# Kernel tuning notes

Measured on AMD Instinct MI355X. Metric: run time of the kernel, lower is better.

## Reference

```python
import jax, jax.numpy as jnp
import numpy as np

B, SEQ, PRED, CIN, COUT = 4, 3584, 512, 7, 7
L = SEQ + PRED              # 4096, divisible by 2*BS -> fit_length is a no-op
D, H, DH, FF, EL = 512, 8, 64, 2048, 2
BS, NHASH = 64, 4           # bucket_size, n_hashes
NB = L // BS                # 64 buckets per hash round
SELF_ATTN_VAL = -5e4        # reformer_pytorch TOKEN_SELF_ATTN_VALUE


def layer_norm(x, g, b, eps=1e-5):
    m = jnp.mean(x, -1, keepdims=True)
    v = jnp.mean((x - m) ** 2, -1, keepdims=True)
    return (x - m) * jax.lax.rsqrt(v + eps) * g + b


def lsh_attention(qk, v, rot):
    # qk, v: (bh, L, DH); rot: (DH, NHASH, NB//2)  (shared across batch & heads)
    bh, Lx, dh = qk.shape
    nb = Lx // BS
    # --- hash vectors ---
    rv = jnp.einsum('btf,fhi->bhti', qk, rot)              # (bh, NHASH, L, nb//2)
    rv = jnp.concatenate([rv, -rv], axis=-1)
    buckets = jnp.argmax(rv, axis=-1)                      # (bh, NHASH, L) int
    buckets = buckets + (jnp.arange(NHASH) * nb)[None, :, None]
    buckets = buckets.reshape(bh, NHASH * Lx)
    ticker = jnp.arange(NHASH * Lx)
    bt = Lx * buckets + (ticker % Lx)[None]                # unique keys
    # --- sort by (bucket, position) ---
    sticker = jnp.argsort(bt, axis=-1)                     # (bh, NHASH*L)
    undo = jnp.argsort(sticker, axis=-1)
    st = sticker % Lx
    sqk = jnp.take_along_axis(qk, st[..., None], axis=1)   # (bh, NHASH*L, DH)
    sv = jnp.take_along_axis(v, st[..., None], axis=1)
    ch = NHASH * nb                                        # number of chunks
    bq_t = st.reshape(bh, ch, BS)
    bqk = sqk.reshape(bh, ch, BS, dh)
    bv = sv.reshape(bh, ch, BS, dh)
    bq = bqk
    nrm = jnp.sqrt(jnp.sum(bqk * bqk, -1, keepdims=True))
    bk = bqk / jnp.maximum(nrm, 1e-12)                     # F.normalize
    def look_one_back(t):
        prev = jnp.concatenate([t[:, -1:], t[:, :-1]], axis=1)
        return jnp.concatenate([t, prev], axis=2)
    bk = look_one_back(bk)
    bvv = look_one_back(bv)
    bkv_t = look_one_back(bq_t)
    dots = jnp.einsum('bcie,bcje->bcij', bq, bk) * (dh ** -0.5)  # (bh, ch, BS, 2BS)
    self_mask = bq_t[..., :, None] == bkv_t[..., None, :]
    dots = jnp.where(self_mask, SELF_ATTN_VAL, dots)
    lse = jax.scipy.special.logsumexp(dots, axis=-1, keepdims=True)
    p = jnp.exp(dots - lse)
    bo = jnp.einsum('bcij,bcje->bcie', p, bvv)
    so = bo.reshape(bh, NHASH * Lx, dh)
    slog = lse.reshape(bh, NHASH * Lx)
    o = jnp.take_along_axis(so, undo[..., None], axis=1)
    logits = jnp.take_along_axis(slog, undo, axis=1)
    o = o.reshape(bh, NHASH, Lx, dh)
    logits = logits.reshape(bh, NHASH, Lx, 1)
    probs = jnp.exp(logits - jax.scipy.special.logsumexp(logits, axis=1, keepdims=True))
    return jnp.sum(o * probs, axis=1)                      # (bh, L, DH)


def lsh_self_attention(x, Wqk, Wv, Wo, bo, rot):
    Bs, Lx, _ = x.shape
    qk = (x @ Wqk).reshape(Bs, Lx, H, DH).transpose(0, 2, 1, 3).reshape(Bs * H, Lx, DH)
    v = (x @ Wv).reshape(Bs, Lx, H, DH).transpose(0, 2, 1, 3).reshape(Bs * H, Lx, DH)
    out = lsh_attention(qk, v, rot)
    out = out.reshape(Bs, H, Lx, DH).transpose(0, 2, 1, 3).reshape(Bs, Lx, D)
    return out @ Wo + bo


def _forward(x_enc, x_dec, x_mark_enc, x_mark_dec, conv_w, month_emb, day_emb,
             weekday_emb, hour_emb, minute_emb, W_qk, W_v, W_out, b_out, rotations,
             ln1_g, ln1_b, W_ff1, b_ff1, W_ff2, b_ff2, ln2_g, ln2_b, lnf_g, lnf_b,
             W_proj, b_proj):
    x = jnp.concatenate([x_enc, x_dec[:, -PRED:, :]], axis=1)            # (B, L, CIN)
    xm = jnp.concatenate([x_mark_enc, x_mark_dec[:, -PRED:, :]], axis=1)
    # TokenEmbedding: Conv1d k=3, circular padding, no bias
    xp = jnp.concatenate([x[:, -1:], x, x[:, :1]], axis=1)
    tok = jax.lax.conv_general_dilated(xp, conv_w, (1,), 'VALID',
                                       dimension_numbers=('NWC', 'WIO', 'NWC'))
    # TemporalEmbedding (freq='t': month/day/weekday/hour/minute)
    temp = (month_emb[xm[..., 0]] + day_emb[xm[..., 1]] + weekday_emb[xm[..., 2]]
            + hour_emb[xm[..., 3]] + minute_emb[xm[..., 4]])
    # PositionalEmbedding (sinusoidal)
    pos = jnp.arange(L, dtype=jnp.float32)[:, None]
    div = jnp.exp(jnp.arange(0, D, 2, dtype=jnp.float32) * (-np.log(10000.0) / D))
    pe = jnp.zeros((L, D), jnp.float32).at[:, 0::2].set(jnp.sin(pos * div)).at[:, 1::2].set(jnp.cos(pos * div))
    h = tok + temp + pe[None]
    for l in range(EL):
        a = lsh_self_attention(h, W_qk[l], W_v[l], W_out[l], b_out[l], rotations[l])
        h = layer_norm(h + a, ln1_g[l], ln1_b[l])
        y = jax.nn.gelu(h @ W_ff1[l] + b_ff1[l], approximate=False)
        y = y @ W_ff2[l] + b_ff2[l]
        h = layer_norm(h + y, ln2_g[l], ln2_b[l])
    h = layer_norm(h, lnf_g, lnf_b)
    return h[:, -PRED:] @ W_proj + b_proj                  # (B, PRED, COUT)


def setup_inputs():
    ks = jax.random.split(jax.random.key(0), 20)
    def n(k, shape, fan_in):
        return jax.random.normal(k, shape, jnp.float32) / np.sqrt(fan_in)
    return {
        'x_enc': jax.random.normal(ks[0], (B, SEQ, CIN), jnp.float32),
        'x_dec': jax.random.normal(ks[1], (B, PRED, CIN), jnp.float32),
        'x_mark_enc': jax.random.randint(ks[2], (B, SEQ, 5), 0, 4, jnp.int32),
        'x_mark_dec': jax.random.randint(ks[3], (B, PRED, 5), 0, 4, jnp.int32),
        'conv_w': n(ks[4], (3, CIN, D), 3 * CIN),
        'month_emb': 0.02 * jax.random.normal(ks[5], (13, D), jnp.float32),
        'day_emb': 0.02 * jax.random.normal(ks[6], (32, D), jnp.float32),
        'weekday_emb': 0.02 * jax.random.normal(ks[7], (7, D), jnp.float32),
        'hour_emb': 0.02 * jax.random.normal(ks[8], (24, D), jnp.float32),
        'minute_emb': 0.02 * jax.random.normal(ks[9], (4, D), jnp.float32),
        'W_qk': n(ks[10], (EL, D, D), D),
        'W_v': n(ks[11], (EL, D, D), D),
        'W_out': n(ks[12], (EL, D, D), D),
        'b_out': jnp.zeros((EL, D), jnp.float32),
        'rotations': jax.random.normal(ks[13], (EL, DH, NHASH, NB // 2), jnp.float32),
        'ln1_g': jnp.ones((EL, D), jnp.float32),
        'ln1_b': jnp.zeros((EL, D), jnp.float32),
        'W_ff1': n(ks[14], (EL, D, FF), D),
        'b_ff1': jnp.zeros((EL, FF), jnp.float32),
        'W_ff2': n(ks[15], (EL, FF, D), FF),
        'b_ff2': jnp.zeros((EL, D), jnp.float32),
        'ln2_g': jnp.ones((EL, D), jnp.float32),
        'ln2_b': jnp.zeros((EL, D), jnp.float32),
        'lnf_g': jnp.ones((D,), jnp.float32),
        'lnf_b': jnp.zeros((D,), jnp.float32),
        'W_proj': n(ks[16], (D, COUT), D),
        'b_proj': jnp.zeros((COUT,), jnp.float32),
    }


def reference(x_enc, x_dec, x_mark_enc, x_mark_dec, conv_w, month_emb, day_emb,
              weekday_emb, hour_emb, minute_emb, W_qk, W_v, W_out, b_out, rotations,
              ln1_g, ln1_b, W_ff1, b_ff1, W_ff2, b_ff2, ln2_g, ln2_b, lnf_g, lnf_b,
              W_proj, b_proj):
    return _forward(x_enc, x_dec, x_mark_enc, x_mark_dec, conv_w, month_emb, day_emb,
                    weekday_emb, hour_emb, minute_emb, W_qk, W_v, W_out, b_out, rotations,
                    ln1_g, ln1_b, W_ff1, b_ff1, W_ff2, b_ff2, ln2_g, ln2_b, lnf_g, lnf_b,
                    W_proj, b_proj)
```

## Files before the change

kernel.cpp:

```cpp
#include <hip/hip_runtime.h>
#include <math.h>


typedef __attribute__((ext_vector_type(8))) __bf16 bf16x8;
typedef __attribute__((ext_vector_type(4))) float floatx4;

__device__ __forceinline__ unsigned short f2bf(float f) {
  union { float f; unsigned int u; } x; x.f = f;
  unsigned int r = x.u + 0x7fffu + ((x.u >> 16) & 1u);
  return (unsigned short)(r >> 16);
}
__device__ __forceinline__ float bf2f(unsigned short u) {
  union { unsigned int u; float f; } x; x.u = ((unsigned int)u) << 16;
  return x.f;
}
__device__ __forceinline__ float gelu_f(float x) {
  return 0.5f * x * (1.0f + erff(x * 0.70710678118654752440f));
}

__global__ __launch_bounds__(256) void pe_kernel(float* __restrict__ pe)
{
  int t = blockIdx.x;
#pragma unroll
  for (int rep = 0; rep < 2; ++rep) {
    int d = threadIdx.x + rep * 256;
    float cf = (float)(-9.210340371976184 / 512.0);
    float xf = (float)(d & ~1) * cf;
    float freq = (float)exp((double)xf);
    float angf = (float)t * freq;
    double a = (double)angf;
    pe[t * 512 + d] = (float)((d & 1) ? cos(a) : sin(a));
  }
}

__global__ __launch_bounds__(256) void embed_kernel(
    const float* __restrict__ x_enc, const float* __restrict__ x_dec,
    const int* __restrict__ xm_enc, const int* __restrict__ xm_dec,
    const float* __restrict__ conv_w,
    const float* __restrict__ month, const float* __restrict__ day,
    const float* __restrict__ wday, const float* __restrict__ hour,
    const float* __restrict__ minute, const float* __restrict__ pe,
    float* __restrict__ h)
{
  int idx = blockIdx.x;
  int b = idx >> 12, t = idx & 4095;
  __shared__ float xv[21];
  __shared__ int mi[5];
  int tid = threadIdx.x;
  if (tid < 21) {
    int w = tid / 7, c = tid % 7;
    int s = (t + w + 4095) & 4095;
    xv[tid] = (s < 3584) ? x_enc[(s + b*3584)*7 + c]
                         : x_dec[((s - 3584) + b*512)*7 + c];
  }
  if (tid >= 32 && tid < 37) {
    int j = tid - 32;
    mi[j] = (t < 3584) ? xm_enc[(b*3584 + t)*5 + j]
                       : xm_dec[(b*512 + (t - 3584))*5 + j];
  }
  __syncthreads();
  int m0 = mi[0], m1 = mi[1], m2 = mi[2], m3 = mi[3], m4 = mi[4];
#pragma unroll
  for (int rep = 0; rep < 2; ++rep) {
    int d = tid + rep*256;
    float tok = 0.f;
#pragma unroll
    for (int wc = 0; wc < 21; ++wc) tok += xv[wc] * conv_w[wc*512 + d];
    float temp = month[m0*512+d] + day[m1*512+d] + wday[m2*512+d]
               + hour[m3*512+d] + minute[m4*512+d];
    h[(size_t)idx*512 + d] = tok + temp + pe[t*512 + d];
  }
}

template<int ACT>
__global__ __launch_bounds__(256) void gemm_kernel(
    const float* __restrict__ A, const float* __restrict__ W,
    const float* __restrict__ bias, float* __restrict__ C,
    int M, int N, int K)
{
  __shared__ float As[8][132];
  __shared__ float Bs[8][132];
  int tid = threadIdx.x;
  int bm = blockIdx.x, bn = blockIdx.y;
  int tr = tid >> 4, tc = tid & 15;
  double acc[8][8];
  float tt[8][8];
#pragma unroll
  for (int i=0;i<8;++i)
#pragma unroll
    for (int j=0;j<8;++j) { acc[i][j]=0.0; tt[i][j]=0.f; }

  int am  = tid >> 1;
  int at  = (tid & 1) * 4;
  int bkr = tid >> 5;
  int bn4 = (tid & 31) * 4;
  const float* Aptr = A + (size_t)(bm*128 + am)*K + at;
  const float* Bptr = W + (size_t)bkr*N + bn*128 + bn4;

  int phase = 0;
  for (int k0 = 0; k0 < K; k0 += 8) {
    float4 a4 = *(const float4*)(Aptr + k0);
    float4 b4 = *(const float4*)(Bptr + (size_t)k0*N);
    __syncthreads();
    As[at+0][am] = a4.x; As[at+1][am] = a4.y;
    As[at+2][am] = a4.z; As[at+3][am] = a4.w;
    *(float4*)&Bs[bkr][bn4] = b4;
    __syncthreads();
#pragma unroll
    for (int k=0;k<8;++k) {
      float4 a0 = *(const float4*)&As[k][tr*8];
      float4 a1 = *(const float4*)&As[k][tr*8+4];
      float4 b0 = *(const float4*)&Bs[k][tc*8];
      float4 b1 = *(const float4*)&Bs[k][tc*8+4];
      float av[8] = {a0.x,a0.y,a0.z,a0.w,a1.x,a1.y,a1.z,a1.w};
      float bv[8] = {b0.x,b0.y,b0.z,b0.w,b1.x,b1.y,b1.z,b1.w};
#pragma unroll
      for (int i=0;i<8;++i)
#pragma unroll
        for (int j=0;j<8;++j) tt[i][j] += av[i]*bv[j];
    }
    phase ^= 1;
    if (!phase) {
#pragma unroll
      for (int i=0;i<8;++i)
#pragma unroll
        for (int j=0;j<8;++j) { acc[i][j] += (double)tt[i][j]; tt[i][j]=0.f; }
    }
  }
  int row0 = bm*128 + tr*8;
  int col0 = bn*128 + tc*8;
  float bvb[8];
#pragma unroll
  for (int j=0;j<8;++j) bvb[j] = bias ? bias[col0+j] : 0.f;
#pragma unroll
  for (int i=0;i<8;++i) {
    float o[8];
#pragma unroll
    for (int j=0;j<8;++j) {
      float vv = (float)acc[i][j] + bvb[j];
      if (ACT==1) vv = gelu_f(vv);
      o[j] = vv;
    }
    float4* dst = (float4*)(C + (size_t)(row0+i)*N + col0);
    dst[0] = make_float4(o[0],o[1],o[2],o[3]);
    dst[1] = make_float4(o[4],o[5],o[6],o[7]);
  }
}

template<int SPLIT>
__global__ __launch_bounds__(256) void wsplit_kernel(
    const float* __restrict__ W, unsigned short* __restrict__ Wt, int K, int N)
{
  __shared__ float tile[32][33];
  int k0 = blockIdx.x*32, n0 = blockIdx.y*32;
  int tid = threadIdx.x;
  int kk = tid >> 3, nn4 = (tid & 7)*4;
  float4 w4 = *(const float4*)(W + (size_t)(k0+kk)*N + n0 + nn4);
  tile[kk][nn4+0]=w4.x; tile[kk][nn4+1]=w4.y;
  tile[kk][nn4+2]=w4.z; tile[kk][nn4+3]=w4.w;
  __syncthreads();
  int n = tid >> 3, k4 = (tid & 7)*4;
  unsigned short o[3][4];
#pragma unroll
  for (int j=0;j<4;++j) {
    float v = tile[k4+j][n];
    unsigned short h0 = f2bf(v);
    float r = v - bf2f(h0);
    unsigned short h1 = f2bf(r);
    o[0][j] = h0; o[1][j] = h1;
    if (SPLIT==3) { float r2 = r - bf2f(h1); o[2][j] = f2bf(r2); }
  }
#pragma unroll
  for (int p=0;p<SPLIT;++p) {
    ushort4* d = (ushort4*)(Wt + (size_t)p*N*K + (size_t)(n0+n)*K + k0 + k4);
    *d = make_ushort4(o[p][0], o[p][1], o[p][2], o[p][3]);
  }
}

template<int SPLIT, int ACT>
__global__ __launch_bounds__(256, 3) void gemm_mfma(
    const float* __restrict__ A, const unsigned short* __restrict__ Wt,
    const float* __restrict__ bias, float* __restrict__ C,
    int M, int N, int K)
{
  constexpr int RS = SPLIT*32 + 8;
  __shared__ __align__(16) unsigned short smem[2*128*RS];
  unsigned short* sA = smem;
  unsigned short* sB = smem + 128*RS;
  float* sE = (float*)smem;

  int tid = threadIdx.x;
  int bm = blockIdx.x, bn = blockIdx.y;
  int lane = tid & 63, wave = tid >> 6;
  int wm = wave & 1, wn = wave >> 1;
  int fr = lane & 15, fk = (lane >> 4) * 8;

  floatx4 acc[4][4];
#pragma unroll
  for (int i=0;i<4;++i)
#pragma unroll
    for (int j=0;j<4;++j) acc[i][j] = (floatx4){0.f,0.f,0.f,0.f};

  int row = tid >> 1, kseg = (tid & 1) * 16;
  const float* aSrc = A + (size_t)(bm*128 + row)*K + kseg;
  const unsigned short* bSrc = Wt + (size_t)(bn*128 + row)*K + kseg;

  float4 av4[4];
  uint4 bv[SPLIT][2];
#pragma unroll
  for (int q=0;q<4;++q) av4[q] = *(const float4*)(aSrc + q*4);
#pragma unroll
  for (int p=0;p<SPLIT;++p) {
    const unsigned short* bp = bSrc + (size_t)p*N*K;
    bv[p][0] = *(const uint4*)(bp);
    bv[p][1] = *(const uint4*)(bp + 8);
  }

  for (int k0 = 0; k0 < K; k0 += 32) {
    __syncthreads();
    unsigned short us[SPLIT][16];
    const float* ff = (const float*)av4;
#pragma unroll
    for (int i=0;i<16;++i) {
      float v = ff[i];
      unsigned short h0 = f2bf(v);
      float r = v - bf2f(h0);
      us[0][i] = h0;
      unsigned short h1 = f2bf(r);
      us[1][i] = h1;
      if (SPLIT==3) { float r2 = r - bf2f(h1); us[2][i] = f2bf(r2); }
    }
#pragma unroll
    for (int p=0;p<SPLIT;++p) {
      uint4* d = (uint4*)&sA[row*RS + p*32 + kseg];
      d[0] = *(const uint4*)&us[p][0];
      d[1] = *(const uint4*)&us[p][8];
      uint4* db = (uint4*)&sB[row*RS + p*32 + kseg];
      db[0] = bv[p][0];
      db[1] = bv[p][1];
    }
    __syncthreads();
    if (k0 + 32 < K) {
#pragma unroll
      for (int q=0;q<4;++q) av4[q] = *(const float4*)(aSrc + k0 + 32 + q*4);
#pragma unroll
      for (int p=0;p<SPLIT;++p) {
        const unsigned short* bp = bSrc + (size_t)p*N*K + k0 + 32;
        bv[p][0] = *(const uint4*)(bp);
        bv[p][1] = *(const uint4*)(bp + 8);
      }
    }

    bf16x8 aF[4][SPLIT];
#pragma unroll
    for (int mt=0;mt<4;++mt)
#pragma unroll
      for (int p=0;p<SPLIT;++p)
        aF[mt][p] = *(const bf16x8*)&sA[(wm*64 + mt*16 + fr)*RS + p*32 + fk];
#pragma unroll
    for (int nt=0;nt<4;++nt) {
      bf16x8 bF[SPLIT];
#pragma unroll
      for (int p=0;p<SPLIT;++p)
        bF[p] = *(const bf16x8*)&sB[(wn*64 + nt*16 + fr)*RS + p*32 + fk];
#pragma unroll
      for (int mt=0;mt<4;++mt) {
        floatx4 c = acc[mt][nt];
        if (SPLIT==3) {
          c = __builtin_amdgcn_mfma_f32_16x16x32_bf16(aF[mt][2], bF[0], c, 0,0,0);
          c = __builtin_amdgcn_mfma_f32_16x16x32_bf16(aF[mt][1], bF[1], c, 0,0,0);
          c = __builtin_amdgcn_mfma_f32_16x16x32_bf16(aF[mt][0], bF[2], c, 0,0,0);
        }
        c = __builtin_amdgcn_mfma_f32_16x16x32_bf16(aF[mt][1], bF[0], c, 0,0,0);
        c = __builtin_amdgcn_mfma_f32_16x16x32_bf16(aF[mt][0], bF[1], c, 0,0,0);
        c = __builtin_amdgcn_mfma_f32_16x16x32_bf16(aF[mt][0], bF[0], c, 0,0,0);
        acc[mt][nt] = c;
      }
    }
  }

  __syncthreads();
#pragma unroll
  for (int half = 0; half < 2; ++half) {
    if (wm == half) {
#pragma unroll
      for (int nt=0;nt<4;++nt) {
        int cl = wn*64 + nt*16 + fr;
        float bb = bias ? bias[bn*128 + cl] : 0.f;
#pragma unroll
        for (int mt=0;mt<4;++mt) {
          int r0 = mt*16 + (lane>>4)*4;
#pragma unroll
          for (int j=0;j<4;++j) {
            float vv = acc[mt][nt][j] + bb;
            if (ACT==1) vv = gelu_f(vv);
            sE[(r0+j)*132 + cl] = vv;
          }
        }
      }
    }
    __syncthreads();
#pragma unroll
    for (int it=0; it<8; ++it) {
      int idx = it*256 + tid;
      int rr = idx >> 5, c4 = (idx & 31) * 4;
      float4 vv = *(const float4*)&sE[rr*132 + c4];
      *(float4*)(C + (size_t)(bm*128 + half*64 + rr)*N + bn*128 + c4) = vv;
    }
    __syncthreads();
  }
}

__global__ __launch_bounds__(256) void hash_kernel(
    const float* __restrict__ qk, const float* __restrict__ rot,
    unsigned char* __restrict__ buckets)
{
  __shared__ float q[2][64];
  __shared__ double rv[2][128];
  int half = threadIdx.x >> 7;
  int lt = threadIdx.x & 127;
  int g = blockIdx.x*2 + half;
  int bh = g >> 12, t = g & 4095;
  int b = bh >> 3, hd = bh & 7;
  if (lt < 64)
    q[half][lt] = qk[((size_t)(b*4096 + t))*512 + hd*64 + lt];
  __syncthreads();
  double acc = 0.0;
#pragma unroll 8
  for (int f=0; f<64; ++f) acc += (double)q[half][f] * (double)rot[f*128 + lt];
  rv[half][lt] = acc;
  __syncthreads();
  if (lt < 4) {
    const double* r = &rv[half][lt*32];
    double best = r[0]; int bi = 0;
#pragma unroll
    for (int j=1; j<64; ++j) {
      double v = (j < 32) ? r[j] : -r[j-32];
      if (v > best) { best = v; bi = j; }
    }
    buckets[((size_t)(bh*4 + lt))*4096 + t] = (unsigned char)bi;
  }
}

__global__ __launch_bounds__(64) void sort_kernel(
    const unsigned char* __restrict__ buckets, int* __restrict__ st)
{
  __shared__ unsigned char sb[4096];
  __shared__ int cnts[64];
  int tid = threadIdx.x;
  const unsigned int* src4 = (const unsigned int*)(buckets + (size_t)blockIdx.x*4096);
  unsigned int* sb4 = (unsigned int*)sb;
  for (int i=tid; i<1024; i+=64) sb4[i] = src4[i];
  __syncthreads();
  unsigned int me = (unsigned int)tid;
  int cnt = 0;
  for (int t4=0; t4<1024; ++t4) {
    unsigned int w = sb4[t4];
    cnt += ((w & 255u) == me) + (((w>>8)&255u) == me)
         + (((w>>16)&255u) == me) + ((w>>24) == me);
  }
  cnts[tid] = cnt;
  __syncthreads();
  int base = 0;
  for (int j=0;j<tid;++j) base += cnts[j];
  int* dst = st + (size_t)blockIdx.x*4096;
  for (int t4=0; t4<1024; ++t4) {
    unsigned int w = sb4[t4];
#pragma unroll
    for (int q=0;q<4;++q)
      if (((w >> (8*q)) & 255u) == me) dst[base++] = t4*4 + q;
  }
}

__global__ __launch_bounds__(256) void attn_kernel(
    const float* __restrict__ qk, const float* __restrict__ v,
    const int* __restrict__ st, float* __restrict__ osc,
    float* __restrict__ logits)
{
  __shared__ float sMem[8704];
  __shared__ float sPT[128][68];
  __shared__ int sPos[128];
  __shared__ float sInv[128];
  int tid = threadIdx.x;
  int bh = blockIdx.x >> 8;
  int c  = blockIdx.x & 255;
  int b = bh >> 3, hd = bh & 7;
  int r = c >> 6;
  if (tid < 128) {
    int cprev = (c + 255) & 255;
    int slot = (tid < 64) ? (c*64 + tid) : (cprev*64 + tid - 64);
    sPos[tid] = st[bh*16384 + slot];
  }
  __syncthreads();
  {
    int j = tid >> 1;
    int f0 = (tid & 1) * 32;
    const float* row = qk + ((size_t)(b*4096 + sPos[j]))*512 + hd*64 + f0;
#pragma unroll
    for (int qq=0; qq<8; ++qq) {
      float4 x = *(const float4*)(row + qq*4);
      int f = f0 + qq*4;
      sMem[(f+0)*132 + j] = x.x;
      sMem[(f+1)*132 + j] = x.y;
      sMem[(f+2)*132 + j] = x.z;
      sMem[(f+3)*132 + j] = x.w;
    }
  }
  __syncthreads();
  if (tid < 128) {
    float s = 0.f;
    for (int f=0; f<64; ++f) { float x = sMem[f*132 + tid]; s += x*x; }
    sInv[tid] = 1.0f / fmaxf(sqrtf(s), 1e-12f);
  }
  __syncthreads();
  int tr = tid >> 4, tcj = tid & 15;
  int i0 = tr*4, j0 = tcj*8;
  float acc[4][8];
#pragma unroll
  for (int i=0;i<4;++i)
#pragma unroll
    for (int j=0;j<8;++j) acc[i][j]=0.f;
  for (int f=0; f<64; ++f) {
    const float* base = &sMem[f*132];
    float4 a  = *(const float4*)(base + i0);
    float4 b0 = *(const float4*)(base + j0);
    float4 b1 = *(const float4*)(base + j0 + 4);
    float av[4] = {a.x,a.y,a.z,a.w};
    float bw[8] = {b0.x,b0.y,b0.z,b0.w,b1.x,b1.y,b1.z,b1.w};
#pragma unroll
    for (int i=0;i<4;++i)
#pragma unroll
      for (int j=0;j<8;++j) acc[i][j] += av[i]*bw[j];
  }
  float inv_j[8]; int pos_j[8];
#pragma unroll
  for (int j=0;j<8;++j) { inv_j[j] = sInv[j0+j]; pos_j[j] = sPos[j0+j]; }
#pragma unroll
  for (int ii=0; ii<4; ++ii) {
    int i = i0 + ii;
    int ipos = sPos[i];
    float dv[8]; float mx = -1e30f;
#pragma unroll
    for (int jj=0;jj<8;++jj) {
      float d = acc[ii][jj] * inv_j[jj] * 0.125f;
      if (pos_j[jj] == ipos) d = -5.0e4f;
      dv[jj] = d; mx = fmaxf(mx, d);
    }
    mx = fmaxf(mx, __shfl_xor(mx, 1, 64));
    mx = fmaxf(mx, __shfl_xor(mx, 2, 64));
    mx = fmaxf(mx, __shfl_xor(mx, 4, 64));
    mx = fmaxf(mx, __shfl_xor(mx, 8, 64));
    float sum = 0.f;
#pragma unroll
    for (int jj=0;jj<8;++jj) sum += expf(dv[jj]-mx);
    sum += __shfl_xor(sum, 1, 64);
    sum += __shfl_xor(sum, 2, 64);
    sum += __shfl_xor(sum, 4, 64);
    sum += __shfl_xor(sum, 8, 64);
    float lse = mx + logf(sum);
    if (tcj == 0)
      logits[((size_t)(bh*4 + r))*4096 + ipos] = lse;
#pragma unroll
    for (int jj=0;jj<8;++jj)
      sPT[j0+jj][i] = expf(dv[jj]-lse);
  }
  __syncthreads();
  {
    int j = tid >> 1;
    int f0 = (tid & 1) * 32;
    const float* row = v + ((size_t)(b*4096 + sPos[j]))*512 + hd*64 + f0;
#pragma unroll
    for (int qq=0; qq<8; ++qq) {
      float4 x = *(const float4*)(row + qq*4);
      *(float4*)&sMem[j*68 + f0 + qq*4] = x;
    }
  }
  __syncthreads();
  int d0 = (tid & 15) * 4;
  float oo[4][4];
#pragma unroll
  for (int i=0;i<4;++i)
#pragma unroll
    for (int j=0;j<4;++j) oo[i][j]=0.f;
  for (int j = 0; j < 128; ++j) {
    float4 pw = *(const float4*)&sPT[j][i0];
    float4 vv = *(const float4*)&sMem[j*68 + d0];
    float pr[4] = {pw.x, pw.y, pw.z, pw.w};
#pragma unroll
    for (int ii=0; ii<4; ++ii) {
      oo[ii][0] += pr[ii]*vv.x;
      oo[ii][1] += pr[ii]*vv.y;
      oo[ii][2] += pr[ii]*vv.z;
      oo[ii][3] += pr[ii]*vv.w;
    }
  }
#pragma unroll
  for (int ii=0; ii<4; ++ii) {
    int pos = sPos[i0+ii];
    float4* dst = (float4*)(osc + (((size_t)(bh*4+r))*4096 + pos)*64 + d0);
    *dst = make_float4(oo[ii][0],oo[ii][1],oo[ii][2],oo[ii][3]);
  }
}

__global__ __launch_bounds__(256) void combine_kernel(
    const float* __restrict__ osc, const float* __restrict__ logits,
    float* __restrict__ merged)
{
  int idx = blockIdx.x;
  int b = idx >> 12, t = idx & 4095;
  int tid = threadIdx.x;
  __shared__ float w[8][4];
  if (tid < 8) {
    size_t lbase = ((size_t)(b*8 + tid)) * 4 * 4096 + t;
    float l0 = logits[lbase], l1 = logits[lbase + 4096],
          l2 = logits[lbase + 8192], l3 = logits[lbase + 12288];
    float m = fmaxf(fmaxf(l0,l1), fmaxf(l2,l3));
    float e0 = expf(l0-m), e1 = expf(l1-m), e2 = expf(l2-m), e3 = expf(l3-m);
    float inv = 1.0f/(e0+e1+e2+e3);
    w[tid][0]=e0*inv; w[tid][1]=e1*inv; w[tid][2]=e2*inv; w[tid][3]=e3*inv;
  }
  __syncthreads();
#pragma unroll
  for (int rep=0; rep<2; ++rep) {
    int d = tid + rep*256;
    int hd = d >> 6, dh = d & 63;
    size_t obase = (((size_t)(b*8 + hd)) * 4 * 4096 + t) * 64 + dh;
    float o = w[hd][0]*osc[obase]
            + w[hd][1]*osc[obase + 262144]
            + w[hd][2]*osc[obase + 524288]
            + w[hd][3]*osc[obase + 786432];
    merged[(size_t)idx*512 + d] = o;
  }
}

__global__ __launch_bounds__(256) void ln_residual_kernel(
    float* __restrict__ h, const float* __restrict__ a,
    const float* __restrict__ g, const float* __restrict__ bb)
{
  int row = blockIdx.x;
  int tid = threadIdx.x;
  size_t base = (size_t)row * 512;
  float x0 = h[base + tid]       + a[base + tid];
  float x1 = h[base + tid + 256] + a[base + tid + 256];
  float s  = x0 + x1;
  float sq = x0*x0 + x1*x1;
#pragma unroll
  for (int off = 32; off > 0; off >>= 1) {
    s  += __shfl_down(s, off, 64);
    sq += __shfl_down(sq, off, 64);
  }
  __shared__ float rs[4], rq[4], sm[2];
  int wv = tid >> 6;
  if ((tid & 63) == 0) { rs[wv] = s; rq[wv] = sq; }
  __syncthreads();
  if (tid == 0) {
    float S = rs[0]+rs[1]+rs[2]+rs[3];
    float Q = rq[0]+rq[1]+rq[2]+rq[3];
    float m = S * (1.0f/512.0f);
    float var = Q * (1.0f/512.0f) - m*m;
    sm[0] = m; sm[1] = rsqrtf(var + 1e-5f);
  }
  __syncthreads();
  float m = sm[0], rstd = sm[1];
  h[base + tid]       = (x0 - m) * rstd * g[tid]       + bb[tid];
  h[base + tid + 256] = (x1 - m) * rstd * g[tid + 256] + bb[tid + 256];
}

__global__ __launch_bounds__(256) void final_kernel(
    const float* __restrict__ h, const float* __restrict__ g, const float* __restrict__ bb,
    const float* __restrict__ Wp, const float* __restrict__ bp, float* __restrict__ out)
{
  int idx = blockIdx.x;
  int b = idx >> 9, tp = idx & 511;
  size_t base = ((size_t)(b*4096 + 3584 + tp)) * 512;
  int tid = threadIdx.x;
  float x0 = h[base + tid], x1 = h[base + tid + 256];
  float s = x0 + x1, sq = x0*x0 + x1*x1;
#pragma unroll
  for (int off = 32; off > 0; off >>= 1) {
    s  += __shfl_down(s, off, 64);
    sq += __shfl_down(sq, off, 64);
  }
  __shared__ float rs[4], rq[4], sm[2];
  int wv = tid >> 6;
  if ((tid & 63) == 0) { rs[wv] = s; rq[wv] = sq; }
  __syncthreads();
  if (tid == 0) {
    float S = rs[0]+rs[1]+rs[2]+rs[3];
    float Q = rq[0]+rq[1]+rq[2]+rq[3];
    float m = S*(1.f/512.f);
    float var = Q*(1.f/512.f) - m*m;
    sm[0]=m; sm[1]=rsqrtf(var+1e-5f);
  }
  __syncthreads();
  __shared__ float xn[512];
  float m = sm[0], rstd = sm[1];
  xn[tid]     = (x0-m)*rstd*g[tid]     + bb[tid];
  xn[tid+256] = (x1-m)*rstd*g[tid+256] + bb[tid+256];
  __syncthreads();
  if (tid < 224) {
    int col = tid >> 5, lane = tid & 31;
    float p = 0.f;
    for (int f = lane; f < 512; f += 32) p += xn[f]*Wp[f*7 + col];
#pragma unroll
    for (int off=16; off>0; off>>=1) p += __shfl_down(p, off, 32);
    if (lane == 0) out[(size_t)idx*7 + col] = p + bp[col];
  }
}

extern "C" void kernel_launch(void* const* d_in, const int* in_sizes, int n_in,
                              void* d_out, int out_size, void* d_ws, size_t ws_size,
                              hipStream_t stream)
{
  (void)in_sizes; (void)n_in; (void)out_size; (void)ws_size;
  const float* x_enc  = (const float*)d_in[0];
  const float* x_dec  = (const float*)d_in[1];
  const int*   xm_enc = (const int*)d_in[2];
  const int*   xm_dec = (const int*)d_in[3];
  const float* conv_w = (const float*)d_in[4];
  const float* month  = (const float*)d_in[5];
  const float* day    = (const float*)d_in[6];
  const float* wday   = (const float*)d_in[7];
  const float* hourE  = (const float*)d_in[8];
  const float* minE   = (const float*)d_in[9];
  const float* W_qk   = (const float*)d_in[10];
  const float* W_v    = (const float*)d_in[11];
  const float* W_out  = (const float*)d_in[12];
  const float* b_out  = (const float*)d_in[13];
  const float* rots   = (const float*)d_in[14];
  const float* ln1_g  = (const float*)d_in[15];
  const float* ln1_b  = (const float*)d_in[16];
  const float* W_ff1  = (const float*)d_in[17];
  const float* b_ff1  = (const float*)d_in[18];
  const float* W_ff2  = (const float*)d_in[19];
  const float* b_ff2  = (const float*)d_in[20];
  const float* ln2_g  = (const float*)d_in[21];
  const float* ln2_b  = (const float*)d_in[22];
  const float* lnf_g  = (const float*)d_in[23];
  const float* lnf_b  = (const float*)d_in[24];
  const float* W_proj = (const float*)d_in[25];
  const float* b_proj = (const float*)d_in[26];

  float* h    = (float*)d_ws;
  float* bufA = h    + 8388608ull;
  float* bufB = bufA + 8388608ull;
  float* osc  = bufB + 8388608ull;
  float* lg   = osc  + 33554432ull;
  int*   stp  = (int*)(lg + 524288ull);
  unsigned char* bkt = (unsigned char*)(stp + 524288ull);
  float* pe   = osc;
  unsigned short* WtA = (unsigned short*)osc;
  unsigned short* WtB = (unsigned short*)bufB;

  pe_kernel<<<4096, 256, 0, stream>>>(pe);
  embed_kernel<<<16384, 256, 0, stream>>>(x_enc, x_dec, xm_enc, xm_dec, conv_w,
                                          month, day, wday, hourE, minE, pe, h);
  for (int l = 0; l < 2; ++l) {
    const float* Wqk = W_qk + (size_t)l*262144;
    const float* Wv  = W_v  + (size_t)l*262144;
    const float* Wo  = W_out+ (size_t)l*262144;
    const float* Wf1 = W_ff1 + (size_t)l*1048576;
    const float* Wf2 = W_ff2 + (size_t)l*1048576;
    const float* rot = rots + (size_t)l*8192;

    gemm_kernel<0><<<dim3(128,4), 256, 0, stream>>>(h, Wqk, nullptr, bufA, 16384, 512, 512);
    if (l == 0) {
      wsplit_kernel<3><<<dim3(16,16), 256, 0, stream>>>(Wv, WtA, 512, 512);
      gemm_mfma<3,0><<<dim3(128,4), 256, 0, stream>>>(h, WtA, nullptr, bufB, 16384, 512, 512);
    } else {
      wsplit_kernel<2><<<dim3(16,16), 256, 0, stream>>>(Wv, WtA, 512, 512);
      gemm_mfma<2,0><<<dim3(128,4), 256, 0, stream>>>(h, WtA, nullptr, bufB, 16384, 512, 512);
    }
    hash_kernel<<<65536, 256, 0, stream>>>(bufA, rot, bkt);
    sort_kernel<<<128, 64, 0, stream>>>(bkt, stp);
    attn_kernel<<<8192, 256, 0, stream>>>(bufA, bufB, stp, osc, lg);
    combine_kernel<<<16384, 256, 0, stream>>>(osc, lg, bufA);
    if (l == 0) {
      wsplit_kernel<3><<<dim3(16,16), 256, 0, stream>>>(Wo, WtA, 512, 512);
      gemm_mfma<3,0><<<dim3(128,4), 256, 0, stream>>>(bufA, WtA, b_out + l*512, bufB, 16384, 512, 512);
    } else {
      wsplit_kernel<2><<<dim3(16,16), 256, 0, stream>>>(Wo, WtA, 512, 512);
      gemm_mfma<2,0><<<dim3(128,4), 256, 0, stream>>>(bufA, WtA, b_out + l*512, bufB, 16384, 512, 512);
    }
    ln_residual_kernel<<<16384, 256, 0, stream>>>(h, bufB, ln1_g + l*512, ln1_b + l*512);
    if (l == 0) {
      wsplit_kernel<3><<<dim3(16,64), 256, 0, stream>>>(Wf1, WtB, 512, 2048);
      gemm_mfma<3,1><<<dim3(128,16), 256, 0, stream>>>(h, WtB, b_ff1 + l*2048, osc, 16384, 2048, 512);
      wsplit_kernel<3><<<dim3(64,16), 256, 0, stream>>>(Wf2, WtB, 2048, 512);
      gemm_mfma<3,0><<<dim3(128,4), 256, 0, stream>>>(osc, WtB, b_ff2 + l*512, bufA, 16384, 512, 2048);
    } else {
      wsplit_kernel<2><<<dim3(16,64), 256, 0, stream>>>(Wf1, WtB, 512, 2048);
      gemm_mfma<2,1><<<dim3(128,16), 256, 0, stream>>>(h, WtB, b_ff1 + l*2048, osc, 16384, 2048, 512);
      wsplit_kernel<2><<<dim3(64,16), 256, 0, stream>>>(Wf2, WtB, 2048, 512);
      gemm_mfma<2,0><<<dim3(128,4), 256, 0, stream>>>(osc, WtB, b_ff2 + l*512, bufA, 16384, 512, 2048);
    }
    ln_residual_kernel<<<16384, 256, 0, stream>>>(h, bufA, ln2_g + l*512, ln2_b + l*512);
  }
  final_kernel<<<2048, 256, 0, stream>>>(h, lnf_g, lnf_b, W_proj, b_proj, (float*)d_out);
}
```

Before: 3.565 ms.

## Pre-split activations into bf16 planes and fuse split output into FF1 GEMM

Adds an asplit kernel that converts fp32 activations into two or three bf16 planes ahead of time, plus a gemm_ps kernel that loads the pre-split A directly. The aim is to drop the per-tile fp32-to-bf16 splitting work inside the GEMM. In layer 1, the FF1 GEMM writes its GELU output straight into split bf16 planes so FF2 can consume them without another split pass. Workspace buffers are remapped to hold the split planes. The cost is extra memory traffic from the standalone split passes, plus the risk of aliasing mistakes in the new buffer layout.

```diff
diff --git a/kernel.cpp b/kernel.cpp
--- a/kernel.cpp
+++ b/kernel.cpp
@@ -174,6 +174,169 @@
   for (int p=0;p<SPLIT;++p) {
     ushort4* d = (ushort4*)(Wt + (size_t)p*N*K + (size_t)(n0+n)*K + k0 + k4);
     *d = make_ushort4(o[p][0], o[p][1], o[p][2], o[p][3]);
+  }
+}
+
+template<int SPLIT>
+__global__ __launch_bounds__(256) void asplit_kernel(
+    const float* __restrict__ A, unsigned short* __restrict__ At, size_t MK)
+{
+  size_t i8 = (((size_t)blockIdx.x)*256 + threadIdx.x) * 8;
+  float4 a0 = *(const float4*)(A + i8);
+  float4 a1 = *(const float4*)(A + i8 + 4);
+  float ff[8] = {a0.x,a0.y,a0.z,a0.w,a1.x,a1.y,a1.z,a1.w};
+  unsigned short u0[8], u1[8], u2[8];
+#pragma unroll
+  for (int i=0;i<8;++i) {
+    float v = ff[i];
+    unsigned short h0 = f2bf(v);
+    float r = v - bf2f(h0);
+    unsigned short h1 = f2bf(r);
+    u0[i] = h0; u1[i] = h1;
+    if (SPLIT==3) { float r2 = r - bf2f(h1); u2[i] = f2bf(r2); }
+  }
+  *(uint4*)(At + i8)        = *(const uint4*)u0;
+  *(uint4*)(At + MK + i8)   = *(const uint4*)u1;
+  if (SPLIT==3) *(uint4*)(At + 2*MK + i8) = *(const uint4*)u2;
+}
+
+template<int SPLIT, int ACT, int OUTP>
+__global__ __launch_bounds__(256, 3) void gemm_ps(
+    const unsigned short* __restrict__ At, const unsigned short* __restrict__ Wt,
+    const float* __restrict__ bias, float* __restrict__ C,
+    int M, int N, int K)
+{
+  constexpr int RS = SPLIT*32 + 8;
+  __shared__ __align__(16) unsigned short smem[2*128*RS];
+  unsigned short* sA = smem;
+  unsigned short* sB = smem + 128*RS;
+  float* sE = (float*)smem;
+
+  int tid = threadIdx.x;
+  int bm = blockIdx.x, bn = blockIdx.y;
+  int lane = tid & 63, wave = tid >> 6;
+  int wm = wave & 1, wn = wave >> 1;
+  int fr = lane & 15, fk = (lane >> 4) * 8;
+
+  floatx4 acc[4][4];
+#pragma unroll
+  for (int i=0;i<4;++i)
+#pragma unroll
+    for (int j=0;j<4;++j) acc[i][j] = (floatx4){0.f,0.f,0.f,0.f};
+
+  int row = tid >> 1, kseg = (tid & 1) * 16;
+  size_t sAp = (size_t)M*K, sBp = (size_t)N*K;
+  const unsigned short* aSrc = At + (size_t)(bm*128 + row)*K + kseg;
+  const unsigned short* bSrc = Wt + (size_t)(bn*128 + row)*K + kseg;
+
+  uint4 av[SPLIT][2], bv[SPLIT][2];
+#pragma unroll
+  for (int p=0;p<SPLIT;++p) {
+    av[p][0] = *(const uint4*)(aSrc + p*sAp);
+    av[p][1] = *(const uint4*)(aSrc + p*sAp + 8);
+    bv[p][0] = *(const uint4*)(bSrc + p*sBp);
+    bv[p][1] = *(const uint4*)(bSrc + p*sBp + 8);
+  }
+
+  for (int k0 = 0; k0 < K; k0 += 32) {
+    __syncthreads();
+#pragma unroll
+    for (int p=0;p<SPLIT;++p) {
+      uint4* da = (uint4*)&sA[row*RS + p*32 + kseg];
+      da[0] = av[p][0]; da[1] = av[p][1];
+      uint4* db = (uint4*)&sB[row*RS + p*32 + kseg];
+      db[0] = bv[p][0]; db[1] = bv[p][1];
+    }
+    __syncthreads();
+    if (k0 + 32 < K) {
+#pragma unroll
+      for (int p=0;p<SPLIT;++p) {
+        av[p][0] = *(const uint4*)(aSrc + p*sAp + k0 + 32);
+        av[p][1] = *(const uint4*)(aSrc + p*sAp + k0 + 40);
+        bv[p][0] = *(const uint4*)(bSrc + p*sBp + k0 + 32);
+        bv[p][1] = *(const uint4*)(bSrc + p*sBp + k0 + 40);
+      }
+    }
+
+    bf16x8 aF[4][SPLIT];
+#pragma unroll
+    for (int mt=0;mt<4;++mt)
+#pragma unroll
+      for (int p=0;p<SPLIT;++p)
+        aF[mt][p] = *(const bf16x8*)&sA[(wm*64 + mt*16 + fr)*RS + p*32 + fk];
+#pragma unroll
+    for (int nt=0;nt<4;++nt) {
+      bf16x8 bF[SPLIT];
+#pragma unroll
+      for (int p=0;p<SPLIT;++p)
+        bF[p] = *(const bf16x8*)&sB[(wn*64 + nt*16 + fr)*RS + p*32 + fk];
+#pragma unroll
+      for (int mt=0;mt<4;++mt) {
+        floatx4 c = acc[mt][nt];
+        if (SPLIT==3) {
+          c = __builtin_amdgcn_mfma_f32_16x16x32_bf16(aF[mt][2], bF[0], c, 0,0,0);
+          c = __builtin_amdgcn_mfma_f32_16x16x32_bf16(aF[mt][1], bF[1], c, 0,0,0);
+          c = __builtin_amdgcn_mfma_f32_16x16x32_bf16(aF[mt][0], bF[2], c, 0,0,0);
+        }
+        c = __builtin_amdgcn_mfma_f32_16x16x32_bf16(aF[mt][1], bF[0], c, 0,0,0);
+        c = __builtin_amdgcn_mfma_f32_16x16x32_bf16(aF[mt][0], bF[1], c, 0,0,0);
+        c = __builtin_amdgcn_mfma_f32_16x16x32_bf16(aF[mt][0], bF[0], c, 0,0,0);
+        acc[mt][nt] = c;
+      }
+    }
+  }
+
+  __syncthreads();
+#pragma unroll
+  for (int half = 0; half < 2; ++half) {
+    if (wm == half) {
+#pragma unroll
+      for (int nt=0;nt<4;++nt) {
+        int cl = wn*64 + nt*16 + fr;
+        float bb = bias ? bias[bn*128 + cl] : 0.f;
+#pragma unroll
+        for (int mt=0;mt<4;++mt) {
+          int r0 = mt*16 + (lane>>4)*4;
+#pragma unroll
+          for (int j=0;j<4;++j) {
+            float vv = acc[mt][nt][j] + bb;
+            if (ACT==1) vv = gelu_f(vv);
+            sE[(r0+j)*132 + cl] = vv;
+          }
+        }
+      }
+    }
+    __syncthreads();
+    if (OUTP == 0) {
+#pragma unroll
+      for (int it=0; it<8; ++it) {
+        int idx = it*256 + tid;
+        int rr = idx >> 5, c4 = (idx & 31) * 4;
+        float4 vv = *(const float4*)&sE[rr*132 + c4];
+        *(float4*)(C + (size_t)(bm*128 + half*64 + rr)*N + bn*128 + c4) = vv;
+      }
+    } else {
+      unsigned short* p0 = (unsigned short*)C;
+      unsigned short* p1 = p0 + (size_t)M*N;
+#pragma unroll
+      for (int it=0; it<8; ++it) {
+        int idx = it*256 + tid;
+        int rr = idx >> 5, c4 = (idx & 31) * 4;
+        float4 vv = *(const float4*)&sE[rr*132 + c4];
+        float fv[4] = {vv.x, vv.y, vv.z, vv.w};
+        unsigned short h0[4], h1[4];
+#pragma unroll
+        for (int j=0;j<4;++j) {
+          unsigned short a = f2bf(fv[j]);
+          float r = fv[j] - bf2f(a);
+          h0[j] = a; h1[j] = f2bf(r);
+        }
+        size_t off = (size_t)(bm*128 + half*64 + rr)*N + bn*128 + c4;
+        *(ushort4*)(p0 + off) = *(const ushort4*)h0;
+        *(ushort4*)(p1 + off) = *(const ushort4*)h1;
+      }
+    }
+    __syncthreads();
   }
 }
 
@@ -642,15 +805,21 @@
   const float* b_proj = (const float*)d_in[26];
 
   float* h    = (float*)d_ws;
-  float* bufA = h    + 8388608ull;
-  float* bufB = bufA + 8388608ull;
-  float* osc  = bufB + 8388608ull;
-  float* lg   = osc  + 33554432ull;
+  float* R1   = h  + 8388608ull;
+  float* R2   = R1 + 8388608ull;
+  float* R3   = R2 + 8388608ull;
+  float* lg   = R3 + 33554432ull;
   int*   stp  = (int*)(lg + 524288ull);
   unsigned char* bkt = (unsigned char*)(stp + 524288ull);
-  float* pe   = osc;
-  unsigned short* WtA = (unsigned short*)osc;
-  unsigned short* WtB = (unsigned short*)bufB;
+
+  float* pe = R3;
+  unsigned short* AhP  = (unsigned short*)R3;
+  unsigned short* WtVO = (unsigned short*)(R3 + 14680064ull);
+  unsigned short* AfP  = (unsigned short*)R1;
+  unsigned short* WtF1 = (unsigned short*)R1 + 26214400ull;
+  unsigned short* WtF2 = (unsigned short*)R1;
+  float* mid = R3;
+  const size_t MKh = 8388608ull;
 
   pe_kernel<<<4096, 256, 0, stream>>>(pe);
   embed_kernel<<<16384, 256, 0, stream>>>(x_enc, x_dec, xm_enc, xm_dec, conv_w,
@@ -663,38 +832,44 @@
     const float* Wf2 = W_ff2 + (size_t)l*1048576;
     const float* rot = rots + (size_t)l*8192;
 
-    gemm_kernel<0><<<dim3(128,4), 256, 0, stream>>>(h, Wqk, nullptr, bufA, 16384, 512, 512);
+    gemm_kernel<0><<<dim3(128,4), 256, 0, stream>>>(h, Wqk, nullptr, R1, 16384, 512, 512);
     if (l == 0) {
-      wsplit_kernel<3><<<dim3(16,16), 256, 0, stream>>>(Wv, WtA, 512, 512);
-      gemm_mfma<3,0><<<dim3(128,4), 256, 0, stream>>>(h, WtA, nullptr, bufB, 16384, 512, 512);
+      asplit_kernel<3><<<4096, 256, 0, stream>>>(h, AhP, MKh);
+      wsplit_kernel<3><<<dim3(16,16), 256, 0, stream>>>(Wv, WtVO, 512, 512);
+      gemm_ps<3,0,0><<<dim3(128,4), 256, 0, stream>>>(AhP, WtVO, nullptr, R2, 16384, 512, 512);
     } else {
-      wsplit_kernel<2><<<dim3(16,16), 256, 0, stream>>>(Wv, WtA, 512, 512);
-      gemm_mfma<2,0><<<dim3(128,4), 256, 0, stream>>>(h, WtA, nullptr, bufB, 16384, 512, 512);
-    }
-    hash_kernel<<<65536, 256, 0, stream>>>(bufA, rot, bkt);
+      asplit_kernel<2><<<4096, 256, 0, stream>>>(h, AhP, MKh);
+      wsplit_kernel<2><<<dim3(16,16), 256, 0, stream>>>(Wv, WtVO, 512, 512);
+      gemm_ps<2,0,0><<<dim3(128,4), 256, 0, stream>>>(AhP, WtVO, nullptr, R2, 16384, 512, 512);
+    }
+    hash_kernel<<<65536, 256, 0, stream>>>(R1, rot, bkt);
     sort_kernel<<<128, 64, 0, stream>>>(bkt, stp);
-    attn_kernel<<<8192, 256, 0, stream>>>(bufA, bufB, stp, osc, lg);
-    combine_kernel<<<16384, 256, 0, stream>>>(osc, lg, bufA);
+    attn_kernel<<<8192, 256, 0, stream>>>(R1, R2, stp, R3, lg);
+    combine_kernel<<<16384, 256, 0, stream>>>(R3, lg, R1);
     if (l == 0) {
-      wsplit_kernel<3><<<dim3(16,16), 256, 0, stream>>>(Wo, WtA, 512, 512);
-      gemm_mfma<3,0><<<dim3(128,4), 256, 0, stream>>>(bufA, WtA, b_out + l*512, bufB, 16384, 512, 512);
+      asplit_kernel<3><<<4096, 256, 0, stream>>>(R1, AhP, MKh);
+      wsplit_kernel<3><<<dim3(16,16), 256, 0, stream>>>(Wo, WtVO, 512, 512);
+      gemm_ps<3,0,0><<<dim3(128,4), 256, 0, stream>>>(AhP, WtVO, b_out + l*512, R2, 16384, 512, 512);
     } else {
-      wsplit_kernel<2><<<dim3(16,16), 256, 0, stream>>>(Wo, WtA, 512, 512);
-      gemm_mfma<2,0><<<dim3(128,4), 256, 0, stream>>>(bufA, WtA, b_out + l*512, bufB, 16384, 512, 512);
-    }
-    ln_residual_kernel<<<16384, 256, 0, stream>>>(h, bufB, ln1_g + l*512, ln1_b + l*512);
+      asplit_kernel<2><<<4096, 256, 0, stream>>>(R1, AhP, MKh);
+      wsplit_kernel<2><<<dim3(16,16), 256, 0, stream>>>(Wo, WtVO, 512, 512);
+      gemm_ps<2,0,0><<<dim3(128,4), 256, 0, stream>>>(AhP, WtVO, b_out + l*512, R2, 16384, 512, 512);
+    }
+    ln_residual_kernel<<<16384, 256, 0, stream>>>(h, R2, ln1_g + l*512, ln1_b + l*512);
     if (l == 0) {
-      wsplit_kernel<3><<<dim3(16,64), 256, 0, stream>>>(Wf1, WtB, 512, 2048);
-      gemm_mfma<3,1><<<dim3(128,16), 256, 0, stream>>>(h, WtB, b_ff1 + l*2048, osc, 16384, 2048, 512);
-      wsplit_kernel<3><<<dim3(64,16), 256, 0, stream>>>(Wf2, WtB, 2048, 512);
-      gemm_mfma<3,0><<<dim3(128,4), 256, 0, stream>>>(osc, WtB, b_ff2 + l*512, bufA, 16384, 512, 2048);
+      asplit_kernel<3><<<4096, 256, 0, stream>>>(h, AfP, MKh);
+      wsplit_kernel<3><<<dim3(16,64), 256, 0, stream>>>(Wf1, WtF1, 512, 2048);
+      gemm_ps<3,1,0><<<dim3(128,16), 256, 0, stream>>>(AfP, WtF1, b_ff1 + l*2048, mid, 16384, 2048, 512);
+      wsplit_kernel<3><<<dim3(64,16), 256, 0, stream>>>(Wf2, WtF2, 2048, 512);
+      gemm_mfma<3,0><<<dim3(128,4), 256, 0, stream>>>(mid, WtF2, b_ff2 + l*512, R2, 16384, 512, 2048);
     } else {
-      wsplit_kernel<2><<<dim3(16,64), 256, 0, stream>>>(Wf1, WtB, 512, 2048);
-      gemm_mfma<2,1><<<dim3(128,16), 256, 0, stream>>>(h, WtB, b_ff1 + l*2048, osc, 16384, 2048, 512);
-      wsplit_kernel<2><<<dim3(64,16), 256, 0, stream>>>(Wf2, WtB, 2048, 512);
-      gemm_mfma<2,0><<<dim3(128,4), 256, 0, stream>>>(osc, WtB, b_ff2 + l*512, bufA, 16384, 512, 2048);
-    }
-    ln_residual_kernel<<<16384, 256, 0, stream>>>(h, bufA, ln2_g + l*512, ln2_b + l*512);
+      asplit_kernel<2><<<4096, 256, 0, stream>>>(h, AfP, MKh);
+      wsplit_kernel<2><<<dim3(16,64), 256, 0, stream>>>(Wf1, WtF1, 512, 2048);
+      gemm_ps<2,1,2><<<dim3(128,16), 256, 0, stream>>>(AfP, WtF1, b_ff1 + l*2048, mid, 16384, 2048, 512);
+      wsplit_kernel<2><<<dim3(64,16), 256, 0, stream>>>(Wf2, WtF2, 2048, 512);
+      gemm_ps<2,0,0><<<dim3(128,4), 256, 0, stream>>>((unsigned short*)mid, WtF2, b_ff2 + l*512, R2, 16384, 512, 2048);
+    }
+    ln_residual_kernel<<<16384, 256, 0, stream>>>(h, R2, ln2_g + l*512, ln2_b + l*512);
   }
   final_kernel<<<2048, 256, 0, stream>>>(h, lnf_g, lnf_b, W_proj, b_proj, (float*)d_out);
 }
```

New measurement: 4.399 ms. 1.23x slower.

## Move LSH bucket attention onto MFMA using split-bf16 emulated fp32

Applied to the files above, without the earlier changes.

Replaces the scalar FP32 QK^T and P·V loops in the bucket attention kernel with 16x16x32 bf16 MFMA instructions, using 2- or 3-term bf16 splits of the operands to approximate fp32 accuracy. Q/K and V rows are now loaded together into registers, and the key norms are computed in registers instead of through a separate shared-memory pass. The aim is to cut ALU-bound inner-product time in a kernel launched 8192 times per layer. In exchange it does extra split and convert work, adds several MFMA passes per product, and may lose slight precision on the P·V path, which uses only 2-term splits.

```diff
diff --git a/kernel.cpp b/kernel.cpp
--- a/kernel.cpp
+++ b/kernel.cpp
@@ -372,133 +372,200 @@
   }
 }
 
-__global__ __launch_bounds__(256) void attn_kernel(
+template<int SQ>
+__global__ __launch_bounds__(256) void attn_mfma(
     const float* __restrict__ qk, const float* __restrict__ v,
     const int* __restrict__ st, float* __restrict__ osc,
     float* __restrict__ logits)
 {
-  __shared__ float sMem[8704];
-  __shared__ float sPT[128][68];
+  constexpr int RQ = 72;
+  constexpr int RP = 136;
+  constexpr int QKE = SQ*128*RQ;
+  constexpr int PVE = 2*64*RP*2;
+  constexpr int UE = (QKE > PVE ? QKE : PVE);
+  __shared__ __align__(16) unsigned short uni[UE];
   __shared__ int sPos[128];
   __shared__ float sInv[128];
+  unsigned short* sQK = uni;
+  unsigned short* sP  = uni;
+  unsigned short* sVT = uni + 2*64*RP;
+
   int tid = threadIdx.x;
   int bh = blockIdx.x >> 8;
   int c  = blockIdx.x & 255;
   int b = bh >> 3, hd = bh & 7;
   int r = c >> 6;
+  int lane = tid & 63, wave = tid >> 6;
+  int fr = lane & 15, fq = lane >> 4;
+  int fk = fq * 8;
+
   if (tid < 128) {
     int cprev = (c + 255) & 255;
     int slot = (tid < 64) ? (c*64 + tid) : (cprev*64 + tid - 64);
     sPos[tid] = st[bh*16384 + slot];
   }
   __syncthreads();
+
+  int row = tid >> 1, ks2 = (tid & 1) * 32;
+  float vreg[32];
   {
-    int j = tid >> 1;
-    int f0 = (tid & 1) * 32;
-    const float* row = qk + ((size_t)(b*4096 + sPos[j]))*512 + hd*64 + f0;
-#pragma unroll
-    for (int qq=0; qq<8; ++qq) {
-      float4 x = *(const float4*)(row + qq*4);
-      int f = f0 + qq*4;
-      sMem[(f+0)*132 + j] = x.x;
-      sMem[(f+1)*132 + j] = x.y;
-      sMem[(f+2)*132 + j] = x.z;
-      sMem[(f+3)*132 + j] = x.w;
-    }
-  }
-  __syncthreads();
-  if (tid < 128) {
-    float s = 0.f;
-    for (int f=0; f<64; ++f) { float x = sMem[f*132 + tid]; s += x*x; }
-    sInv[tid] = 1.0f / fmaxf(sqrtf(s), 1e-12f);
-  }
-  __syncthreads();
-  int tr = tid >> 4, tcj = tid & 15;
-  int i0 = tr*4, j0 = tcj*8;
-  float acc[4][8];
-#pragma unroll
-  for (int i=0;i<4;++i)
-#pragma unroll
-    for (int j=0;j<8;++j) acc[i][j]=0.f;
-  for (int f=0; f<64; ++f) {
-    const float* base = &sMem[f*132];
-    float4 a  = *(const float4*)(base + i0);
-    float4 b0 = *(const float4*)(base + j0);
-    float4 b1 = *(const float4*)(base + j0 + 4);
-    float av[4] = {a.x,a.y,a.z,a.w};
-    float bw[8] = {b0.x,b0.y,b0.z,b0.w,b1.x,b1.y,b1.z,b1.w};
-#pragma unroll
-    for (int i=0;i<4;++i)
-#pragma unroll
-      for (int j=0;j<8;++j) acc[i][j] += av[i]*bw[j];
-  }
-  float inv_j[8]; int pos_j[8];
-#pragma unroll
-  for (int j=0;j<8;++j) { inv_j[j] = sInv[j0+j]; pos_j[j] = sPos[j0+j]; }
-#pragma unroll
-  for (int ii=0; ii<4; ++ii) {
-    int i = i0 + ii;
-    int ipos = sPos[i];
-    float dv[8]; float mx = -1e30f;
-#pragma unroll
-    for (int jj=0;jj<8;++jj) {
-      float d = acc[ii][jj] * inv_j[jj] * 0.125f;
-      if (pos_j[jj] == ipos) d = -5.0e4f;
-      dv[jj] = d; mx = fmaxf(mx, d);
-    }
-    mx = fmaxf(mx, __shfl_xor(mx, 1, 64));
-    mx = fmaxf(mx, __shfl_xor(mx, 2, 64));
-    mx = fmaxf(mx, __shfl_xor(mx, 4, 64));
-    mx = fmaxf(mx, __shfl_xor(mx, 8, 64));
-    float sum = 0.f;
-#pragma unroll
-    for (int jj=0;jj<8;++jj) sum += expf(dv[jj]-mx);
-    sum += __shfl_xor(sum, 1, 64);
-    sum += __shfl_xor(sum, 2, 64);
-    sum += __shfl_xor(sum, 4, 64);
-    sum += __shfl_xor(sum, 8, 64);
-    float lse = mx + logf(sum);
-    if (tcj == 0)
-      logits[((size_t)(bh*4 + r))*4096 + ipos] = lse;
-#pragma unroll
-    for (int jj=0;jj<8;++jj)
-      sPT[j0+jj][i] = expf(dv[jj]-lse);
-  }
-  __syncthreads();
-  {
-    int j = tid >> 1;
-    int f0 = (tid & 1) * 32;
-    const float* row = v + ((size_t)(b*4096 + sPos[j]))*512 + hd*64 + f0;
-#pragma unroll
-    for (int qq=0; qq<8; ++qq) {
-      float4 x = *(const float4*)(row + qq*4);
-      *(float4*)&sMem[j*68 + f0 + qq*4] = x;
-    }
-  }
-  __syncthreads();
-  int d0 = (tid & 15) * 4;
-  float oo[4][4];
-#pragma unroll
-  for (int i=0;i<4;++i)
-#pragma unroll
-    for (int j=0;j<4;++j) oo[i][j]=0.f;
-  for (int j = 0; j < 128; ++j) {
-    float4 pw = *(const float4*)&sPT[j][i0];
-    float4 vv = *(const float4*)&sMem[j*68 + d0];
-    float pr[4] = {pw.x, pw.y, pw.z, pw.w};
-#pragma unroll
-    for (int ii=0; ii<4; ++ii) {
-      oo[ii][0] += pr[ii]*vv.x;
-      oo[ii][1] += pr[ii]*vv.y;
-      oo[ii][2] += pr[ii]*vv.z;
-      oo[ii][3] += pr[ii]*vv.w;
-    }
-  }
-#pragma unroll
-  for (int ii=0; ii<4; ++ii) {
-    int pos = sPos[i0+ii];
-    float4* dst = (float4*)(osc + (((size_t)(bh*4+r))*4096 + pos)*64 + d0);
-    *dst = make_float4(oo[ii][0],oo[ii][1],oo[ii][2],oo[ii][3]);
+    size_t rbase = ((size_t)(b*4096 + sPos[row]))*512 + hd*64 + ks2;
+    const float* src  = qk + rbase;
+    const float* vsrc = v  + rbase;
+    float qreg[32];
+    float ss = 0.f;
+#pragma unroll
+    for (int i=0;i<32;i+=4) {
+      float4 x = *(const float4*)(src + i);
+      qreg[i]=x.x; qreg[i+1]=x.y; qreg[i+2]=x.z; qreg[i+3]=x.w;
+      ss += x.x*x.x + x.y*x.y + x.z*x.z + x.w*x.w;
+      float4 y = *(const float4*)(vsrc + i);
+      vreg[i]=y.x; vreg[i+1]=y.y; vreg[i+2]=y.z; vreg[i+3]=y.w;
+    }
+    ss += __shfl_xor(ss, 1, 64);
+    if ((tid & 1) == 0) sInv[row] = 1.0f / fmaxf(sqrtf(ss), 1e-12f);
+    unsigned short us[3][32];
+#pragma unroll
+    for (int i=0;i<32;++i) {
+      float vv = qreg[i];
+      unsigned short h0 = f2bf(vv);
+      float r1 = vv - bf2f(h0);
+      unsigned short h1 = f2bf(r1);
+      us[0][i] = h0; us[1][i] = h1;
+      if (SQ==3) { float r2 = r1 - bf2f(h1); us[2][i] = f2bf(r2); }
+    }
+#pragma unroll
+    for (int p=0;p<SQ;++p) {
+      uint4* d = (uint4*)&sQK[p*128*RQ + row*RQ + ks2];
+      d[0] = *(const uint4*)&us[p][0];
+      d[1] = *(const uint4*)&us[p][8];
+      d[2] = *(const uint4*)&us[p][16];
+      d[3] = *(const uint4*)&us[p][24];
+    }
+  }
+  __syncthreads();
+
+  floatx4 s[8];
+#pragma unroll
+  for (int nt=0;nt<8;++nt) s[nt] = (floatx4){0.f,0.f,0.f,0.f};
+#pragma unroll
+  for (int ks=0; ks<2; ++ks) {
+    bf16x8 aQ[SQ];
+#pragma unroll
+    for (int p=0;p<SQ;++p)
+      aQ[p] = *(const bf16x8*)&sQK[p*128*RQ + (wave*16 + fr)*RQ + ks*32 + fk];
+#pragma unroll
+    for (int nt=0;nt<8;++nt) {
+      bf16x8 bK[SQ];
+#pragma unroll
+      for (int p=0;p<SQ;++p)
+        bK[p] = *(const bf16x8*)&sQK[p*128*RQ + (nt*16 + fr)*RQ + ks*32 + fk];
+      floatx4 cc = s[nt];
+      if (SQ==3) {
+        cc = __builtin_amdgcn_mfma_f32_16x16x32_bf16(aQ[2], bK[0], cc, 0,0,0);
+        cc = __builtin_amdgcn_mfma_f32_16x16x32_bf16(aQ[1], bK[1], cc, 0,0,0);
+        cc = __builtin_amdgcn_mfma_f32_16x16x32_bf16(aQ[0], bK[2], cc, 0,0,0);
+      }
+      cc = __builtin_amdgcn_mfma_f32_16x16x32_bf16(aQ[1], bK[0], cc, 0,0,0);
+      cc = __builtin_amdgcn_mfma_f32_16x16x32_bf16(aQ[0], bK[1], cc, 0,0,0);
+      cc = __builtin_amdgcn_mfma_f32_16x16x32_bf16(aQ[0], bK[0], cc, 0,0,0);
+      s[nt] = cc;
+    }
+  }
+
+  int ipos[4];
+#pragma unroll
+  for (int reg=0;reg<4;++reg) ipos[reg] = sPos[wave*16 + fq*4 + reg];
+  float dv[8][4];
+  float mx[4] = {-1e30f,-1e30f,-1e30f,-1e30f};
+#pragma unroll
+  for (int nt=0;nt<8;++nt) {
+    float invj = sInv[nt*16 + fr];
+    int jpos = sPos[nt*16 + fr];
+#pragma unroll
+    for (int reg=0;reg<4;++reg) {
+      float d = s[nt][reg] * invj * 0.125f;
+      if (jpos == ipos[reg]) d = -5.0e4f;
+      dv[nt][reg] = d;
+      mx[reg] = fmaxf(mx[reg], d);
+    }
+  }
+#pragma unroll
+  for (int reg=0;reg<4;++reg) {
+    mx[reg] = fmaxf(mx[reg], __shfl_xor(mx[reg], 1, 64));
+    mx[reg] = fmaxf(mx[reg], __shfl_xor(mx[reg], 2, 64));
+    mx[reg] = fmaxf(mx[reg], __shfl_xor(mx[reg], 4, 64));
+    mx[reg] = fmaxf(mx[reg], __shfl_xor(mx[reg], 8, 64));
+  }
+  float sum[4] = {0.f,0.f,0.f,0.f};
+#pragma unroll
+  for (int nt=0;nt<8;++nt)
+#pragma unroll
+    for (int reg=0;reg<4;++reg) sum[reg] += expf(dv[nt][reg] - mx[reg]);
+  float lse[4];
+#pragma unroll
+  for (int reg=0;reg<4;++reg) {
+    sum[reg] += __shfl_xor(sum[reg], 1, 64);
+    sum[reg] += __shfl_xor(sum[reg], 2, 64);
+    sum[reg] += __shfl_xor(sum[reg], 4, 64);
+    sum[reg] += __shfl_xor(sum[reg], 8, 64);
+    lse[reg] = mx[reg] + logf(sum[reg]);
+  }
+  if (fr == 0) {
+#pragma unroll
+    for (int reg=0;reg<4;++reg)
+      logits[((size_t)(bh*4 + r))*4096 + ipos[reg]] = lse[reg];
+  }
+#pragma unroll
+  for (int nt=0;nt<8;++nt)
+#pragma unroll
+    for (int reg=0;reg<4;++reg) dv[nt][reg] = expf(dv[nt][reg] - lse[reg]);
+
+  __syncthreads();
+
+#pragma unroll
+  for (int nt=0;nt<8;++nt) {
+    int key = nt*16 + fr;
+#pragma unroll
+    for (int reg=0;reg<4;++reg) {
+      int m = wave*16 + fq*4 + reg;
+      float p = dv[nt][reg];
+      unsigned short h0 = f2bf(p);
+      sP[0*64*RP + m*RP + key] = h0;
+      sP[1*64*RP + m*RP + key] = f2bf(p - bf2f(h0));
+    }
+  }
+#pragma unroll
+  for (int i=0;i<32;++i) {
+    int dh = ks2 + i;
+    float vv = vreg[i];
+    unsigned short h0 = f2bf(vv);
+    sVT[0*64*RP + dh*RP + row] = h0;
+    sVT[1*64*RP + dh*RP + row] = f2bf(vv - bf2f(h0));
+  }
+  __syncthreads();
+
+  size_t obase = ((size_t)(bh*4 + r)) * 4096;
+#pragma unroll
+  for (int dt=0;dt<4;++dt) {
+    floatx4 o = (floatx4){0.f,0.f,0.f,0.f};
+#pragma unroll
+    for (int ks=0; ks<4; ++ks) {
+      bf16x8 aP0 = *(const bf16x8*)&sP[0*64*RP + (wave*16 + fr)*RP + ks*32 + fk];
+      bf16x8 aP1 = *(const bf16x8*)&sP[1*64*RP + (wave*16 + fr)*RP + ks*32 + fk];
+      bf16x8 bV0 = *(const bf16x8*)&sVT[0*64*RP + (dt*16 + fr)*RP + ks*32 + fk];
+      bf16x8 bV1 = *(const bf16x8*)&sVT[1*64*RP + (dt*16 + fr)*RP + ks*32 + fk];
+      o = __builtin_amdgcn_mfma_f32_16x16x32_bf16(aP1, bV1, o, 0,0,0);
+      o = __builtin_amdgcn_mfma_f32_16x16x32_bf16(aP1, bV0, o, 0,0,0);
+      o = __builtin_amdgcn_mfma_f32_16x16x32_bf16(aP0, bV1, o, 0,0,0);
+      o = __builtin_amdgcn_mfma_f32_16x16x32_bf16(aP0, bV0, o, 0,0,0);
+    }
+    int dh = dt*16 + fr;
+#pragma unroll
+    for (int reg=0;reg<4;++reg) {
+      int m = wave*16 + fq*4 + reg;
+      osc[(obase + sPos[m])*64 + dh] = o[reg];
+    }
   }
 }
 
@@ -673,7 +740,10 @@
     }
     hash_kernel<<<65536, 256, 0, stream>>>(bufA, rot, bkt);
     sort_kernel<<<128, 64, 0, stream>>>(bkt, stp);
-    attn_kernel<<<8192, 256, 0, stream>>>(bufA, bufB, stp, osc, lg);
+    if (l == 0)
+      attn_mfma<3><<<8192, 256, 0, stream>>>(bufA, bufB, stp, osc, lg);
+    else
+      attn_mfma<2><<<8192, 256, 0, stream>>>(bufA, bufB, stp, osc, lg);
     combine_kernel<<<16384, 256, 0, stream>>>(osc, lg, bufA);
     if (l == 0) {
       wsplit_kernel<3><<<dim3(16,16), 256, 0, stream>>>(Wo, WtA, 512, 512);
```

After: 3.342 ms, median of 2. 6.3% less time.
